# Kernel optimization log

Measured on AMD Instinct MI355X. Metric: run time of the kernel, lower is better.

## Reference

```python
import jax, jax.numpy as jnp
import numpy as np

MARGIN = 0.3   # init margin
NUMBER = 1024  # OHEM: number of hardest losses to mine
N, D = 8192, 128


def setup_inputs() -> dict:
    key = jax.random.key(0)
    k1, k2 = jax.random.split(key)
    pair1 = jax.random.normal(k1, (N, D), dtype=jnp.float32)
    pair2 = jax.random.normal(k2, (N, D), dtype=jnp.float32)
    return {"pair1": pair1, "pair2": pair2}


def _pairwise_losses(pair1, pair2):
    # d[i, j] = ||pair1[i] - pair2[j]||^2 via GEMM expansion
    sq1 = jnp.sum(pair1 * pair1, axis=1)            # [N]
    sq2 = jnp.sum(pair2 * pair2, axis=1)            # [N]
    cross = pair1 @ pair2.T                          # [N, N]
    d = sq1[:, None] + sq2[None, :] - 2.0 * cross    # [N, N]
    dist_ap = jnp.diagonal(d)                        # [N], ||pair1[i]-pair2[i]||^2
    loss = jax.nn.relu(dist_ap[:, None] - d + MARGIN)  # [N, N]
    offdiag = ~jnp.eye(d.shape[0], dtype=bool)       # i == j is skipped
    return loss, offdiag


def reference(pair1, pair2):
    loss, offdiag = _pairwise_losses(pair1, pair2)
    n = loss.shape[0]
    cnt = 2 * n * (n - 1)  # original appends each (i, j) loss twice
    # all_loss: mean over all 2*N*(N-1) (duplicated) losses
    all_loss = 2.0 * jnp.sum(jnp.where(offdiag, loss, 0.0)) / cnt
    # OHEM: top NUMBER losses over the duplicated candidate set
    flat = jnp.where(offdiag, loss, -1.0).ravel()    # sentinel -1 masks diagonal
    flat2 = jnp.concatenate([flat, flat])            # each loss appears twice
    topv, _ = jax.lax.top_k(flat2, NUMBER)
    pos = topv > 0.0
    avg_num = jnp.sum(pos)
    avg_sum = jnp.sum(jnp.where(pos, topv, 0.0))
    # if no positive loss among the mined set, fall back to the single largest loss
    avg_loss = jnp.where(avg_num > 0, avg_sum / jnp.maximum(avg_num, 1).astype(topv.dtype), topv[0])
    return avg_loss, all_loss
```

## Files before the change

kernel.cpp:

```cpp
#include <hip/hip_runtime.h>
#include <stdint.h>


#define NROWS 8192
#define DDIM  128
#define MARGIN_F 0.3f
#define HALFK 512
#define SUBCAP 8192
#define SHIST_BINS 1024

typedef unsigned short u16;
typedef short bf16x8 __attribute__((ext_vector_type(8)));
typedef float f32x4 __attribute__((ext_vector_type(4)));

#define OFF_P1B  0
#define OFF_P2B  (2*1024*1024)
#define OFF_AARR (4*1024*1024)
#define OFF_BARR (OFF_AARR + 32768)
#define OFF_MISC (OFF_AARR + 65536)
#define OFF_CAND (OFF_MISC + 8192)

__global__ void init_kernel(int* zbase) {
    const int n = 1232;
    for (int i = threadIdx.x; i < n; i += blockDim.x) zbase[i] = 0;
}

__device__ __forceinline__ u16 f2bf(float f) {
    unsigned int u = __float_as_uint(f);
    u = (u + 0x7FFFu + ((u >> 16) & 1u)) >> 16;
    return (u16)u;
}
__device__ __forceinline__ float bf2f(u16 u) {
    return __uint_as_float(((unsigned int)u) << 16);
}

__global__ __launch_bounds__(256) void prep_kernel(
    const float* __restrict__ p1, const float* __restrict__ p2,
    u16* __restrict__ p1b, u16* __restrict__ p2b,
    float* __restrict__ aArr, float* __restrict__ bArr)
{
    const int wid = threadIdx.x >> 6, lane = threadIdx.x & 63;
    const int row = blockIdx.x*4 + wid;
    const float2 v1 = *(const float2*)&p1[row*DDIM + lane*2];
    const float2 v2 = *(const float2*)&p2[row*DDIM + lane*2];
    p1b[row*DDIM + lane*2]     = f2bf(v1.x);
    p1b[row*DDIM + lane*2 + 1] = f2bf(v1.y);
    p2b[row*DDIM + lane*2]     = f2bf(v2.x);
    p2b[row*DDIM + lane*2 + 1] = f2bf(v2.y);
    float sq = v2.x*v2.x + v2.y*v2.y;
    float cp = v1.x*v2.x + v1.y*v2.y;
    #pragma unroll
    for (int off = 32; off > 0; off >>= 1) {
        sq += __shfl_down(sq, off);
        cp += __shfl_down(cp, off);
    }
    if (lane == 0) {
        bArr[row] = sq;
        aArr[row] = sq - 2.0f*cp + MARGIN_F;
    }
}

__global__ __launch_bounds__(256) void sample_kernel(
    const u16* __restrict__ p1b, const u16* __restrict__ p2b,
    const float* __restrict__ aArr, const float* __restrict__ bArr,
    int* __restrict__ shist)
{
    __shared__ float p1row[DDIM];
    __shared__ int h[SHIST_BINS];
    const int b = blockIdx.x;
    const int i = (b >> 3)*1024 + 512;
    const int j0 = (b & 7)*1024;
    const int tid = threadIdx.x;
    for (int k = tid; k < SHIST_BINS; k += 256) h[k] = 0;
    if (tid < DDIM) p1row[tid] = bf2f(p1b[i*DDIM + tid]);
    __syncthreads();
    const float ai = aArr[i];
    #pragma unroll
    for (int jj = 0; jj < 4; ++jj) {
        const int j = j0 + jj*256 + tid;
        const u16* prow = &p2b[j*DDIM];
        float dot = 0.f;
        for (int k = 0; k < DDIM; k += 8) {
            uint4 q = *(const uint4*)&prow[k];
            const u16* e = (const u16*)&q;
            #pragma unroll
            for (int t = 0; t < 8; ++t) dot += p1row[k + t] * bf2f(e[t]);
        }
        float v = ai - bArr[j] + 2.0f*dot;
        if (j != i && v > 0.f) {
            int bin = (int)(v * 4.0f);
            if (bin > SHIST_BINS - 1) bin = SHIST_BINS - 1;
            atomicAdd(&h[bin], 1);
        }
    }
    __syncthreads();
    for (int k = tid; k < SHIST_BINS; k += 256) if (h[k]) atomicAdd(&shist[k], h[k]);
}

__global__ void pick_kernel(const int* __restrict__ shist, float* __restrict__ Tv) {
    if (threadIdx.x == 0) {
        int run = 0, b;
        float t = 0.f;
        for (b = SHIST_BINS - 1; b >= 0; --b) { run += shist[b]; if (run >= 8) break; }
        if (run >= 8) {
            if (b < 0) b = 0;
            while (run > 24 && run - shist[b] >= 8 && b < SHIST_BINS - 1) { run -= shist[b]; b++; }
            t = 0.25f * (float)b;
        }
        *Tv = t;
    }
}

__global__ __launch_bounds__(256, 2) void pair_gemm(
    const u16* __restrict__ p1b, const u16* __restrict__ p2b,
    const float* __restrict__ aArr, const float* __restrict__ bArr,
    const float* __restrict__ Tv,
    float* __restrict__ pS, int* __restrict__ pP,
    int* __restrict__ candCnt, float* __restrict__ cand)
{
    __shared__ u16 At[128][136];
    __shared__ u16 Bt[128][136];
    __shared__ float sredS[4];
    __shared__ int   sredP[4];
    const int tid = threadIdx.x;
    const int bi = blockIdx.y, bj = blockIdx.x;
    const int i0 = bi*128, j0 = bj*128;
    const float T0 = *Tv;
    #pragma unroll
    for (int it = 0; it < 8; ++it) {
        int c = tid + it*256;
        int r = c >> 4, cc = (c & 15) * 8;
        *(uint4*)&At[r][cc] = *(const uint4*)&p1b[(i0 + r)*DDIM + cc];
        *(uint4*)&Bt[r][cc] = *(const uint4*)&p2b[(j0 + r)*DDIM + cc];
    }
    __syncthreads();
    const int lane = tid & 63, wid = tid >> 6;
    const int r16 = lane & 15, hi = lane >> 4;
    const int wm = (wid >> 1)*64, wn = (wid & 1)*64;
    f32x4 acc[4][4];
    #pragma unroll
    for (int a = 0; a < 4; ++a)
        #pragma unroll
        for (int b = 0; b < 4; ++b) acc[a][b] = (f32x4){0.f, 0.f, 0.f, 0.f};
    #pragma unroll
    for (int ks = 0; ks < 4; ++ks) {
        const int kc = ks*32 + hi*8;
        bf16x8 aF[4], bF[4];
        #pragma unroll
        for (int mi = 0; mi < 4; ++mi) aF[mi] = *(const bf16x8*)&At[wm + mi*16 + r16][kc];
        #pragma unroll
        for (int ni = 0; ni < 4; ++ni) bF[ni] = *(const bf16x8*)&Bt[wn + ni*16 + r16][kc];
        #pragma unroll
        for (int mi = 0; mi < 4; ++mi)
            #pragma unroll
            for (int ni = 0; ni < 4; ++ni)
                acc[mi][ni] = __builtin_amdgcn_mfma_f32_16x16x32_bf16(aF[mi], bF[ni], acc[mi][ni], 0, 0, 0);
    }
    float bv[4], av[4][4];
    #pragma unroll
    for (int ni = 0; ni < 4; ++ni) bv[ni] = bArr[j0 + wn + ni*16 + r16];
    #pragma unroll
    for (int mi = 0; mi < 4; ++mi)
        #pragma unroll
        for (int r = 0; r < 4; ++r) av[mi][r] = aArr[i0 + wm + mi*16 + hi*4 + r];
    const int copy = (bi ^ bj) & 63;
    int*   myCnt  = &candCnt[copy];
    float* myCand = &cand[(size_t)copy * SUBCAP];
    float lsum = 0.f; int pcnt = 0;
    #pragma unroll
    for (int mi = 0; mi < 4; ++mi) {
        #pragma unroll
        for (int ni = 0; ni < 4; ++ni) {
            const bool hasDiag = (i0 + wm + mi*16) == (j0 + wn + ni*16);
            #pragma unroll
            for (int r = 0; r < 4; ++r) {
                const float v = av[mi][r] - bv[ni] + 2.0f*acc[mi][ni][r];
                lsum += fmaxf(v, 0.f);
                pcnt += (v > 0.f) ? 1 : 0;
                bool ok = (v >= T0);
                if (hasDiag && (hi*4 + r) == r16) ok = false;
                if (ok) {
                    int idx = atomicAdd(myCnt, 1);
                    if (idx < SUBCAP) myCand[idx] = v;
                }
            }
        }
    }
    #pragma unroll
    for (int off = 32; off > 0; off >>= 1) {
        lsum += __shfl_down(lsum, off);
        pcnt += __shfl_down(pcnt, off);
    }
    if (lane == 0) { sredS[wid] = lsum; sredP[wid] = pcnt; }
    __syncthreads();
    if (tid == 0) {
        atomicAdd(&pS[copy], sredS[0] + sredS[1] + sredS[2] + sredS[3]);
        atomicAdd(&pP[copy], sredP[0] + sredP[1] + sredP[2] + sredP[3]);
    }
}

__device__ __forceinline__ float block_reduce1024(float v, float* red, int tid) {
    #pragma unroll
    for (int off = 32; off > 0; off >>= 1) v += __shfl_down(v, off);
    __syncthreads();
    if ((tid & 63) == 0) red[tid >> 6] = v;
    __syncthreads();
    if (tid == 0) {
        float t = 0.f;
        #pragma unroll
        for (int w = 0; w < 16; ++w) t += red[w];
        red[0] = t;
    }
    __syncthreads();
    return red[0];
}

__global__ __launch_bounds__(1024) void select_kernel(
    const float* __restrict__ pS, const int* __restrict__ pP,
    const int* __restrict__ candCnt, const float* __restrict__ cand,
    const float* __restrict__ Tv, float* __restrict__ out)
{
    __shared__ int h1[1024];
    __shared__ int h2[1024];
    __shared__ float red[16];
    __shared__ int ints[8];
    __shared__ float fl[2];
    __shared__ float lst[4096];
    const int tid = threadIdx.x;
    for (int k = tid; k < 1024; k += 1024) { h1[k] = 0; h2[k] = 0; }
    if (tid == 0) {
        double sd = 0.0; int p = 0, c = 0;
        for (int k = 0; k < 64; ++k) {
            sd += (double)pS[k];
            p += pP[k];
            int cc = candCnt[k];
            c += (cc > SUBCAP ? SUBCAP : cc);
        }
        sd -= (double)NROWS * (double)MARGIN_F;
        if (sd < 0.0) sd = 0.0;
        p -= NROWS;
        if (p < 0) p = 0;
        ints[0] = p; ints[1] = c; ints[6] = 0;
        fl[0] = (float)sd;
    }
    __syncthreads();
    const int P = ints[0], C = ints[1];
    const float S = fl[0];
    const float all_loss = S * (1.0f / 67100672.0f);
    const float lo = *Tv;
    float avg = 0.f;

    if (P == 0) {
        avg = 0.f;
    } else if (P < HALFK) {
        avg = S / (float)P;
    } else if (C < HALFK) {
        float s = 0.f;
        for (int c = 0; c < 64; ++c) {
            int n = min(candCnt[c], SUBCAP);
            for (int k = tid; k < n; k += 1024) s += cand[(size_t)c*SUBCAP + k];
        }
        s = block_reduce1024(s, red, tid);
        avg = (C > 0) ? (s + (float)(HALFK - C)*lo) / (float)HALFK : 0.f;
    } else {
        for (int c = 0; c < 64; ++c) {
            int n = min(candCnt[c], SUBCAP);
            for (int k = tid; k < n; k += 1024) {
                float v = cand[(size_t)c*SUBCAP + k];
                int b = (int)((v - lo) * 0.25f);
                b = b < 0 ? 0 : (b > 1023 ? 1023 : b);
                atomicAdd(&h1[b], 1);
            }
        }
        __syncthreads();
        if (tid == 0) {
            int run = 0;
            for (int b = 1023; b >= 0; --b) {
                run += h1[b];
                if (run >= HALFK) { ints[2] = b; ints[3] = HALFK - (run - h1[b]); break; }
            }
        }
        __syncthreads();
        const int b1 = ints[2], needK = ints[3];
        const float lo2 = lo + (float)b1 * 4.0f;
        float s1 = 0.f;
        for (int c = 0; c < 64; ++c) {
            int n = min(candCnt[c], SUBCAP);
            for (int k = tid; k < n; k += 1024) {
                float v = cand[(size_t)c*SUBCAP + k];
                int b = (int)((v - lo) * 0.25f);
                b = b < 0 ? 0 : (b > 1023 ? 1023 : b);
                if (b > b1) s1 += v;
                else if (b == b1) {
                    int sb = (int)((v - lo2) * 256.0f);
                    sb = sb < 0 ? 0 : (sb > 1023 ? 1023 : sb);
                    atomicAdd(&h2[sb], 1);
                }
            }
        }
        s1 = block_reduce1024(s1, red, tid);
        if (tid == 0) {
            int run = 0;
            for (int b = 1023; b >= 0; --b) {
                run += h2[b];
                if (run >= needK) { ints[4] = b; ints[5] = needK - (run - h2[b]); break; }
            }
        }
        __syncthreads();
        const int b2 = ints[4], need3 = ints[5];
        float s2 = 0.f;
        for (int c = 0; c < 64; ++c) {
            int n = min(candCnt[c], SUBCAP);
            for (int k = tid; k < n; k += 1024) {
                float v = cand[(size_t)c*SUBCAP + k];
                int b = (int)((v - lo) * 0.25f);
                b = b < 0 ? 0 : (b > 1023 ? 1023 : b);
                if (b == b1) {
                    int sb = (int)((v - lo2) * 256.0f);
                    sb = sb < 0 ? 0 : (sb > 1023 ? 1023 : sb);
                    if (sb > b2) s2 += v;
                    else if (sb == b2) {
                        int idx = atomicAdd(&ints[6], 1);
                        if (idx < 4096) lst[idx] = v;
                    }
                }
            }
        }
        s2 = block_reduce1024(s2, red, tid);
        __syncthreads();
        const int m = min(ints[6], 4096);
        float s3 = 0.f;
        for (int k = tid; k < m; k += 1024) {
            float v = lst[k]; int g = 0;
            for (int j = 0; j < m; ++j) {
                float u = lst[j];
                g += (u > v) || (u == v && j < k);
            }
            if (g < need3) s3 += v;
        }
        s3 = block_reduce1024(s3, red, tid);
        avg = (s1 + s2 + s3) * (1.0f / (float)HALFK);
    }
    if (tid == 0) { out[0] = avg; out[1] = all_loss; }
}

extern "C" void kernel_launch(void* const* d_in, const int* in_sizes, int n_in,
                              void* d_out, int out_size, void* d_ws, size_t ws_size,
                              hipStream_t stream)
{
    const float* p1 = (const float*)d_in[0];
    const float* p2 = (const float*)d_in[1];
    char* ws = (char*)d_ws;
    u16*   p1b  = (u16*)(ws + OFF_P1B);
    u16*   p2b  = (u16*)(ws + OFF_P2B);
    float* aArr = (float*)(ws + OFF_AARR);
    float* bArr = (float*)(ws + OFF_BARR);
    int*   misc = (int*)(ws + OFF_MISC);
    int*   shist = misc;
    float* pS   = (float*)(misc + 1024);
    int*   pP   = misc + 1088;
    int*   cCnt = misc + 1152;
    float* Tv   = (float*)(misc + 1216);
    float* cand = (float*)(ws + OFF_CAND);
    float* out  = (float*)d_out;

    init_kernel<<<1, 256, 0, stream>>>(misc);
    prep_kernel<<<NROWS/4, 256, 0, stream>>>(p1, p2, p1b, p2b, aArr, bArr);
    sample_kernel<<<64, 256, 0, stream>>>(p1b, p2b, aArr, bArr, shist);
    pick_kernel<<<1, 64, 0, stream>>>(shist, Tv);
    dim3 grid(64, 64);
    pair_gemm<<<grid, 256, 0, stream>>>(p1b, p2b, aArr, bArr, Tv, pS, pP, cCnt, cand);
    select_kernel<<<1, 1024, 0, stream>>>(pS, pP, cCnt, cand, Tv, out);
}
```

Baseline: 401.8 us.

## Split pair GEMM into candidate and sum kernels; use wave-aggregated atomics

After: 425.2 us. 5.8% more time.

```diff
diff --git a/kernel.cpp b/kernel.cpp
--- a/kernel.cpp
+++ b/kernel.cpp
@@ -97,26 +97,117 @@
     for (int k = tid; k < SHIST_BINS; k += 256) if (h[k]) atomicAdd(&shist[k], h[k]);
 }
 
-__global__ void pick_kernel(const int* __restrict__ shist, float* __restrict__ Tv) {
-    if (threadIdx.x == 0) {
-        int run = 0, b;
-        float t = 0.f;
-        for (b = SHIST_BINS - 1; b >= 0; --b) { run += shist[b]; if (run >= 8) break; }
-        if (run >= 8) {
-            if (b < 0) b = 0;
-            while (run > 24 && run - shist[b] >= 8 && b < SHIST_BINS - 1) { run -= shist[b]; b++; }
-            t = 0.25f * (float)b;
-        }
-        *Tv = t;
-    }
-}
-
-__global__ __launch_bounds__(256, 2) void pair_gemm(
+__global__ __launch_bounds__(256) void pick_kernel(
+    const int* __restrict__ shist, float* __restrict__ Tv)
+{
+    __shared__ int h[SHIST_BINS];
+    __shared__ int chunk[256];
+    const int tid = threadIdx.x;
+    #pragma unroll
+    for (int k = 0; k < 4; ++k) h[tid + k*256] = shist[tid + k*256];
+    __syncthreads();
+    int cs = 0;
+    #pragma unroll
+    for (int k = 0; k < 4; ++k) cs += h[tid*4 + k];
+    chunk[tid] = cs;
+    __syncthreads();
+    if (tid == 0) {
+        int run = 0, tc = -1;
+        for (int t = 255; t >= 0; --t) {
+            if (run + chunk[t] >= 8) { tc = t; break; }
+            run += chunk[t];
+        }
+        float t0 = 0.f;
+        if (tc >= 0) {
+            int b = tc*4 + 3;
+            for (; b >= tc*4; --b) { run += h[b]; if (run >= 8) break; }
+            if (b < tc*4) b = tc*4;
+            while (run > 24 && run - h[b] >= 8 && b < SHIST_BINS - 1) { run -= h[b]; b++; }
+            t0 = 0.25f * (float)b;
+        }
+        *Tv = t0;
+    }
+}
+
+__global__ __launch_bounds__(256, 2) void gemm_cand(
     const u16* __restrict__ p1b, const u16* __restrict__ p2b,
     const float* __restrict__ aArr, const float* __restrict__ bArr,
     const float* __restrict__ Tv,
-    float* __restrict__ pS, int* __restrict__ pP,
     int* __restrict__ candCnt, float* __restrict__ cand)
+{
+    __shared__ u16 At[128][136];
+    __shared__ u16 Bt[128][136];
+    const int tid = threadIdx.x;
+    const int bi = blockIdx.y, bj = blockIdx.x;
+    const int i0 = bi*128, j0 = bj*128;
+    const float T0 = *Tv;
+    #pragma unroll
+    for (int it = 0; it < 8; ++it) {
+        int c = tid + it*256;
+        int r = c >> 4, cc = (c & 15) * 8;
+        *(uint4*)&At[r][cc] = *(const uint4*)&p1b[(i0 + r)*DDIM + cc];
+        *(uint4*)&Bt[r][cc] = *(const uint4*)&p2b[(j0 + r)*DDIM + cc];
+    }
+    __syncthreads();
+    const int lane = tid & 63, wid = tid >> 6;
+    const int r16 = lane & 15, hi = lane >> 4;
+    const int wm = (wid >> 1)*64, wn = (wid & 1)*64;
+    f32x4 acc[4][4];
+    #pragma unroll
+    for (int a = 0; a < 4; ++a)
+        #pragma unroll
+        for (int b = 0; b < 4; ++b) acc[a][b] = (f32x4){0.f, 0.f, 0.f, 0.f};
+    #pragma unroll
+    for (int ks = 0; ks < 4; ++ks) {
+        const int kc = ks*32 + hi*8;
+        bf16x8 aF[4], bF[4];
+        #pragma unroll
+        for (int mi = 0; mi < 4; ++mi) aF[mi] = *(const bf16x8*)&At[wm + mi*16 + r16][kc];
+        #pragma unroll
+        for (int ni = 0; ni < 4; ++ni) bF[ni] = *(const bf16x8*)&Bt[wn + ni*16 + r16][kc];
+        #pragma unroll
+        for (int mi = 0; mi < 4; ++mi)
+            #pragma unroll
+            for (int ni = 0; ni < 4; ++ni)
+                acc[mi][ni] = __builtin_amdgcn_mfma_f32_16x16x32_bf16(aF[mi], bF[ni], acc[mi][ni], 0, 0, 0);
+    }
+    float bv[4], av[4][4];
+    #pragma unroll
+    for (int ni = 0; ni < 4; ++ni) bv[ni] = bArr[j0 + wn + ni*16 + r16];
+    #pragma unroll
+    for (int mi = 0; mi < 4; ++mi)
+        #pragma unroll
+        for (int r = 0; r < 4; ++r) av[mi][r] = aArr[i0 + wm + mi*16 + hi*4 + r];
+    const int copy = (bi ^ bj) & 63;
+    #pragma unroll
+    for (int mi = 0; mi < 4; ++mi) {
+        #pragma unroll
+        for (int ni = 0; ni < 4; ++ni) {
+            #pragma unroll
+            for (int r = 0; r < 4; ++r) {
+                const int ii = i0 + wm + mi*16 + hi*4 + r;
+                const int jj = j0 + wn + ni*16 + r16;
+                const float v = av[mi][r] - bv[ni] + 2.0f*acc[mi][ni][r];
+                const bool cd = (v > 0.f) && (ii != jj) && (v >= T0);
+                unsigned long long m = __ballot(cd);
+                if (m) {
+                    int base = 0;
+                    if (lane == 0) base = atomicAdd(&candCnt[copy], __popcll(m));
+                    base = __shfl(base, 0);
+                    if (cd) {
+                        int pos = base + __popcll(m & ((1ULL << lane) - 1));
+                        if (pos < SUBCAP) cand[(size_t)copy*SUBCAP + pos] = v;
+                    }
+                }
+            }
+        }
+    }
+}
+
+__global__ __launch_bounds__(256, 2) void gemm_sum(
+    const u16* __restrict__ p1b, const u16* __restrict__ p2b,
+    const float* __restrict__ aArr, const float* __restrict__ bArr,
+    float* __restrict__ pS, int* __restrict__ pP)
 {
     __shared__ u16 At[128][136];
     __shared__ u16 Bt[128][136];
@@ -125,7 +216,6 @@
     const int tid = threadIdx.x;
     const int bi = blockIdx.y, bj = blockIdx.x;
     const int i0 = bi*128, j0 = bj*128;
-    const float T0 = *Tv;
     #pragma unroll
     for (int it = 0; it < 8; ++it) {
         int c = tid + it*256;
@@ -163,29 +253,22 @@
     for (int mi = 0; mi < 4; ++mi)
         #pragma unroll
         for (int r = 0; r < 4; ++r) av[mi][r] = aArr[i0 + wm + mi*16 + hi*4 + r];
-    const int copy = (bi ^ bj) & 63;
-    int*   myCnt  = &candCnt[copy];
-    float* myCand = &cand[(size_t)copy * SUBCAP];
-    float lsum = 0.f; int pcnt = 0;
+    float ls[4] = {0.f, 0.f, 0.f, 0.f};
+    int   pc[4] = {0, 0, 0, 0};
     #pragma unroll
     for (int mi = 0; mi < 4; ++mi) {
         #pragma unroll
         for (int ni = 0; ni < 4; ++ni) {
-            const bool hasDiag = (i0 + wm + mi*16) == (j0 + wn + ni*16);
             #pragma unroll
             for (int r = 0; r < 4; ++r) {
                 const float v = av[mi][r] - bv[ni] + 2.0f*acc[mi][ni][r];
-                lsum += fmaxf(v, 0.f);
-                pcnt += (v > 0.f) ? 1 : 0;
-                bool ok = (v >= T0);
-                if (hasDiag && (hi*4 + r) == r16) ok = false;
-                if (ok) {
-                    int idx = atomicAdd(myCnt, 1);
-                    if (idx < SUBCAP) myCand[idx] = v;
-                }
-            }
-        }
-    }
+                ls[r] += fmaxf(v, 0.f);
+                pc[r] += (v > 0.f) ? 1 : 0;
+            }
+        }
+    }
+    float lsum = (ls[0] + ls[1]) + (ls[2] + ls[3]);
+    int   pcnt = (pc[0] + pc[1]) + (pc[2] + pc[3]);
     #pragma unroll
     for (int off = 32; off > 0; off >>= 1) {
         lsum += __shfl_down(lsum, off);
@@ -194,6 +277,7 @@
     if (lane == 0) { sredS[wid] = lsum; sredP[wid] = pcnt; }
     __syncthreads();
     if (tid == 0) {
+        const int copy = (bi ^ bj) & 63;
         atomicAdd(&pS[copy], sredS[0] + sredS[1] + sredS[2] + sredS[3]);
         atomicAdd(&pP[copy], sredP[0] + sredP[1] + sredP[2] + sredP[3]);
     }
@@ -367,8 +451,9 @@
     init_kernel<<<1, 256, 0, stream>>>(misc);
     prep_kernel<<<NROWS/4, 256, 0, stream>>>(p1, p2, p1b, p2b, aArr, bArr);
     sample_kernel<<<64, 256, 0, stream>>>(p1b, p2b, aArr, bArr, shist);
-    pick_kernel<<<1, 64, 0, stream>>>(shist, Tv);
+    pick_kernel<<<1, 256, 0, stream>>>(shist, Tv);
     dim3 grid(64, 64);
-    pair_gemm<<<grid, 256, 0, stream>>>(p1b, p2b, aArr, bArr, Tv, pS, pP, cCnt, cand);
+    gemm_cand<<<grid, 256, 0, stream>>>(p1b, p2b, aArr, bArr, Tv, cCnt, cand);
+    gemm_sum<<<grid, 256, 0, stream>>>(p1b, p2b, aArr, bArr, pS, pP);
     select_kernel<<<1, 1024, 0, stream>>>(pS, pP, cCnt, cand, Tv, out);
 }
```

## Restructure pairwise GEMM to register-resident B tile streaming A rows without LDS

Applied to the files above, without the earlier changes.

New measurement: 527.1 us. +31.2%, slower.

```diff
diff --git a/kernel.cpp b/kernel.cpp
--- a/kernel.cpp
+++ b/kernel.cpp
@@ -97,105 +97,138 @@
     for (int k = tid; k < SHIST_BINS; k += 256) if (h[k]) atomicAdd(&shist[k], h[k]);
 }
 
-__global__ void pick_kernel(const int* __restrict__ shist, float* __restrict__ Tv) {
-    if (threadIdx.x == 0) {
-        int run = 0, b;
-        float t = 0.f;
-        for (b = SHIST_BINS - 1; b >= 0; --b) { run += shist[b]; if (run >= 8) break; }
-        if (run >= 8) {
-            if (b < 0) b = 0;
-            while (run > 24 && run - shist[b] >= 8 && b < SHIST_BINS - 1) { run -= shist[b]; b++; }
-            t = 0.25f * (float)b;
-        }
-        *Tv = t;
-    }
-}
-
-__global__ __launch_bounds__(256, 2) void pair_gemm(
+__global__ __launch_bounds__(256) void pick_kernel(
+    const int* __restrict__ shist, float* __restrict__ Tv)
+{
+    __shared__ int h[SHIST_BINS];
+    __shared__ int chunk[256];
+    const int tid = threadIdx.x;
+    #pragma unroll
+    for (int k = 0; k < 4; ++k) h[tid + k*256] = shist[tid + k*256];
+    __syncthreads();
+    int cs = 0;
+    #pragma unroll
+    for (int k = 0; k < 4; ++k) cs += h[tid*4 + k];
+    chunk[tid] = cs;
+    __syncthreads();
+    if (tid == 0) {
+        int run = 0, tc = -1;
+        for (int t = 255; t >= 0; --t) {
+            if (run + chunk[t] >= 8) { tc = t; break; }
+            run += chunk[t];
+        }
+        float t0 = 0.f;
+        if (tc >= 0) {
+            int b = tc*4 + 3;
+            for (; b >= tc*4; --b) { run += h[b]; if (run >= 8) break; }
+            if (b < tc*4) b = tc*4;
+            while (run > 24 && run - h[b] >= 8 && b < SHIST_BINS - 1) { run -= h[b]; b++; }
+            t0 = 0.25f * (float)b;
+        }
+        *Tv = t0;
+    }
+}
+
+__global__ __launch_bounds__(512, 2) void pair_main(
     const u16* __restrict__ p1b, const u16* __restrict__ p2b,
     const float* __restrict__ aArr, const float* __restrict__ bArr,
     const float* __restrict__ Tv,
     float* __restrict__ pS, int* __restrict__ pP,
     int* __restrict__ candCnt, float* __restrict__ cand)
 {
-    __shared__ u16 At[128][136];
-    __shared__ u16 Bt[128][136];
-    __shared__ float sredS[4];
-    __shared__ int   sredP[4];
     const int tid = threadIdx.x;
-    const int bi = blockIdx.y, bj = blockIdx.x;
-    const int i0 = bi*128, j0 = bj*128;
+    const int w = tid >> 6, lane = tid & 63;
+    const int r16 = lane & 15, hi = lane >> 4;
+    const int j0 = blockIdx.x * 64;
+    const int ibase = blockIdx.y * 2048;
     const float T0 = *Tv;
-    #pragma unroll
-    for (int it = 0; it < 8; ++it) {
-        int c = tid + it*256;
-        int r = c >> 4, cc = (c & 15) * 8;
-        *(uint4*)&At[r][cc] = *(const uint4*)&p1b[(i0 + r)*DDIM + cc];
-        *(uint4*)&Bt[r][cc] = *(const uint4*)&p2b[(j0 + r)*DDIM + cc];
-    }
-    __syncthreads();
-    const int lane = tid & 63, wid = tid >> 6;
-    const int r16 = lane & 15, hi = lane >> 4;
-    const int wm = (wid >> 1)*64, wn = (wid & 1)*64;
-    f32x4 acc[4][4];
-    #pragma unroll
-    for (int a = 0; a < 4; ++a)
-        #pragma unroll
-        for (int b = 0; b < 4; ++b) acc[a][b] = (f32x4){0.f, 0.f, 0.f, 0.f};
-    #pragma unroll
-    for (int ks = 0; ks < 4; ++ks) {
-        const int kc = ks*32 + hi*8;
-        bf16x8 aF[4], bF[4];
-        #pragma unroll
-        for (int mi = 0; mi < 4; ++mi) aF[mi] = *(const bf16x8*)&At[wm + mi*16 + r16][kc];
-        #pragma unroll
-        for (int ni = 0; ni < 4; ++ni) bF[ni] = *(const bf16x8*)&Bt[wn + ni*16 + r16][kc];
-        #pragma unroll
-        for (int mi = 0; mi < 4; ++mi)
+    const char* Ap = (const char*)p1b;
+    const char* Bp = (const char*)p2b;
+
+    bf16x8 bF[4][4];
+    #pragma unroll
+    for (int ni = 0; ni < 4; ++ni) {
+        const int j = j0 + ni*16 + r16;
+        #pragma unroll
+        for (int ks = 0; ks < 4; ++ks)
+            bF[ni][ks] = *(const bf16x8*)(Bp + (size_t)j*256 + hi*16 + ks*64);
+    }
+    float bv[4];
+    int jj[4];
+    #pragma unroll
+    for (int ni = 0; ni < 4; ++ni) {
+        jj[ni] = j0 + ni*16 + r16;
+        bv[ni] = bArr[jj[ni]];
+    }
+
+    float ls[4] = {0.f, 0.f, 0.f, 0.f};
+    int pcnt = 0;
+    const int copy = (blockIdx.x*8 + w) & 63;
+    int*   myCnt  = &candCnt[copy];
+    float* myCand = &cand[(size_t)copy * SUBCAP];
+
+    const int row0 = ibase + w*256;
+
+    bf16x8 aCur[4];
+    float avCur[4];
+    #pragma unroll
+    for (int ks = 0; ks < 4; ++ks)
+        aCur[ks] = *(const bf16x8*)(Ap + (size_t)(row0 + r16)*256 + hi*16 + ks*64);
+    #pragma unroll
+    for (int r = 0; r < 4; ++r) avCur[r] = aArr[row0 + hi*4 + r];
+
+    #pragma unroll
+    for (int t = 0; t < 16; ++t) {
+        bf16x8 aNxt[4];
+        float avNxt[4];
+        if (t < 15) {
+            const int rn = row0 + (t + 1)*16;
+            #pragma unroll
+            for (int ks = 0; ks < 4; ++ks)
+                aNxt[ks] = *(const bf16x8*)(Ap + (size_t)(rn + r16)*256 + hi*16 + ks*64);
+            #pragma unroll
+            for (int r = 0; r < 4; ++r) avNxt[r] = aArr[rn + hi*4 + r];
+        }
+        f32x4 acc[4];
+        #pragma unroll
+        for (int ni = 0; ni < 4; ++ni) acc[ni] = (f32x4){0.f, 0.f, 0.f, 0.f};
+        #pragma unroll
+        for (int ks = 0; ks < 4; ++ks)
             #pragma unroll
             for (int ni = 0; ni < 4; ++ni)
-                acc[mi][ni] = __builtin_amdgcn_mfma_f32_16x16x32_bf16(aF[mi], bF[ni], acc[mi][ni], 0, 0, 0);
-    }
-    float bv[4], av[4][4];
-    #pragma unroll
-    for (int ni = 0; ni < 4; ++ni) bv[ni] = bArr[j0 + wn + ni*16 + r16];
-    #pragma unroll
-    for (int mi = 0; mi < 4; ++mi)
-        #pragma unroll
-        for (int r = 0; r < 4; ++r) av[mi][r] = aArr[i0 + wm + mi*16 + hi*4 + r];
-    const int copy = (bi ^ bj) & 63;
-    int*   myCnt  = &candCnt[copy];
-    float* myCand = &cand[(size_t)copy * SUBCAP];
-    float lsum = 0.f; int pcnt = 0;
-    #pragma unroll
-    for (int mi = 0; mi < 4; ++mi) {
+                acc[ni] = __builtin_amdgcn_mfma_f32_16x16x32_bf16(aCur[ks], bF[ni][ks], acc[ni], 0, 0, 0);
+        const int rr = row0 + t*16;
+        const int iL = rr + hi*4;
         #pragma unroll
         for (int ni = 0; ni < 4; ++ni) {
-            const bool hasDiag = (i0 + wm + mi*16) == (j0 + wn + ni*16);
             #pragma unroll
             for (int r = 0; r < 4; ++r) {
-                const float v = av[mi][r] - bv[ni] + 2.0f*acc[mi][ni][r];
-                lsum += fmaxf(v, 0.f);
+                const float v = avCur[r] - bv[ni] + 2.0f*acc[ni][r];
+                ls[ni] += fmaxf(v, 0.f);
                 pcnt += (v > 0.f) ? 1 : 0;
-                bool ok = (v >= T0);
-                if (hasDiag && (hi*4 + r) == r16) ok = false;
-                if (ok) {
+                const bool isD = (iL + r) == jj[ni];
+                const float vc = isD ? -1e30f : v;
+                if (vc >= T0) {
                     int idx = atomicAdd(myCnt, 1);
                     if (idx < SUBCAP) myCand[idx] = v;
                 }
             }
         }
-    }
+        #pragma unroll
+        for (int ks = 0; ks < 4; ++ks) aCur[ks] = aNxt[ks];
+        #pragma unroll
+        for (int r = 0; r < 4; ++r) avCur[r] = avNxt[r];
+    }
+
+    float lsum = (ls[0] + ls[1]) + (ls[2] + ls[3]);
     #pragma unroll
     for (int off = 32; off > 0; off >>= 1) {
         lsum += __shfl_down(lsum, off);
         pcnt += __shfl_down(pcnt, off);
     }
-    if (lane == 0) { sredS[wid] = lsum; sredP[wid] = pcnt; }
-    __syncthreads();
-    if (tid == 0) {
-        atomicAdd(&pS[copy], sredS[0] + sredS[1] + sredS[2] + sredS[3]);
-        atomicAdd(&pP[copy], sredP[0] + sredP[1] + sredP[2] + sredP[3]);
+    if (lane == 0) {
+        atomicAdd(&pS[copy], lsum);
+        atomicAdd(&pP[copy], pcnt);
     }
 }
 
@@ -367,8 +400,8 @@
     init_kernel<<<1, 256, 0, stream>>>(misc);
     prep_kernel<<<NROWS/4, 256, 0, stream>>>(p1, p2, p1b, p2b, aArr, bArr);
     sample_kernel<<<64, 256, 0, stream>>>(p1b, p2b, aArr, bArr, shist);
-    pick_kernel<<<1, 64, 0, stream>>>(shist, Tv);
-    dim3 grid(64, 64);
-    pair_gemm<<<grid, 256, 0, stream>>>(p1b, p2b, aArr, bArr, Tv, pS, pP, cCnt, cand);
+    pick_kernel<<<1, 256, 0, stream>>>(shist, Tv);
+    dim3 grid(128, 4);
+    pair_main<<<grid, 512, 0, stream>>>(p1b, p2b, aArr, bArr, Tv, pS, pP, cCnt, cand);
     select_kernel<<<1, 1024, 0, stream>>>(pS, pP, cCnt, cand, Tv, out);
 }
```

## Enlarge pair GEMM tile to 256x256 with 512 threads and parallelize threshold pick

Applied to the files above, without the earlier changes.

Measured after the change: 382.4 us. -4.8%, faster.

```diff
diff --git a/kernel.cpp b/kernel.cpp
--- a/kernel.cpp
+++ b/kernel.cpp
@@ -97,38 +97,56 @@
     for (int k = tid; k < SHIST_BINS; k += 256) if (h[k]) atomicAdd(&shist[k], h[k]);
 }
 
-__global__ void pick_kernel(const int* __restrict__ shist, float* __restrict__ Tv) {
-    if (threadIdx.x == 0) {
-        int run = 0, b;
-        float t = 0.f;
-        for (b = SHIST_BINS - 1; b >= 0; --b) { run += shist[b]; if (run >= 8) break; }
-        if (run >= 8) {
-            if (b < 0) b = 0;
-            while (run > 24 && run - shist[b] >= 8 && b < SHIST_BINS - 1) { run -= shist[b]; b++; }
-            t = 0.25f * (float)b;
-        }
-        *Tv = t;
-    }
-}
-
-__global__ __launch_bounds__(256, 2) void pair_gemm(
+__global__ __launch_bounds__(256) void pick_kernel(
+    const int* __restrict__ shist, float* __restrict__ Tv)
+{
+    __shared__ int h[SHIST_BINS];
+    __shared__ int chunk[256];
+    const int tid = threadIdx.x;
+    #pragma unroll
+    for (int k = 0; k < 4; ++k) h[tid + k*256] = shist[tid + k*256];
+    __syncthreads();
+    int cs = 0;
+    #pragma unroll
+    for (int k = 0; k < 4; ++k) cs += h[tid*4 + k];
+    chunk[tid] = cs;
+    __syncthreads();
+    if (tid == 0) {
+        int run = 0, tc = -1;
+        for (int t = 255; t >= 0; --t) {
+            if (run + chunk[t] >= 8) { tc = t; break; }
+            run += chunk[t];
+        }
+        float t0 = 0.f;
+        if (tc >= 0) {
+            int b = tc*4 + 3;
+            for (; b >= tc*4; --b) { run += h[b]; if (run >= 8) break; }
+            if (b < tc*4) b = tc*4;
+            while (run > 24 && run - h[b] >= 8 && b < SHIST_BINS - 1) { run -= h[b]; b++; }
+            t0 = 0.25f * (float)b;
+        }
+        *Tv = t0;
+    }
+}
+
+__global__ __launch_bounds__(512, 1) void pair_gemm(
     const u16* __restrict__ p1b, const u16* __restrict__ p2b,
     const float* __restrict__ aArr, const float* __restrict__ bArr,
     const float* __restrict__ Tv,
     float* __restrict__ pS, int* __restrict__ pP,
     int* __restrict__ candCnt, float* __restrict__ cand)
 {
-    __shared__ u16 At[128][136];
-    __shared__ u16 Bt[128][136];
-    __shared__ float sredS[4];
-    __shared__ int   sredP[4];
+    __shared__ u16 At[256][136];
+    __shared__ u16 Bt[256][136];
+    __shared__ float sredS[8];
+    __shared__ int   sredP[8];
     const int tid = threadIdx.x;
     const int bi = blockIdx.y, bj = blockIdx.x;
-    const int i0 = bi*128, j0 = bj*128;
+    const int i0 = bi*256, j0 = bj*256;
     const float T0 = *Tv;
     #pragma unroll
     for (int it = 0; it < 8; ++it) {
-        int c = tid + it*256;
+        int c = tid + it*512;
         int r = c >> 4, cc = (c & 15) * 8;
         *(uint4*)&At[r][cc] = *(const uint4*)&p1b[(i0 + r)*DDIM + cc];
         *(uint4*)&Bt[r][cc] = *(const uint4*)&p2b[(j0 + r)*DDIM + cc];
@@ -136,56 +154,64 @@
     __syncthreads();
     const int lane = tid & 63, wid = tid >> 6;
     const int r16 = lane & 15, hi = lane >> 4;
-    const int wm = (wid >> 1)*64, wn = (wid & 1)*64;
-    f32x4 acc[4][4];
-    #pragma unroll
-    for (int a = 0; a < 4; ++a)
-        #pragma unroll
-        for (int b = 0; b < 4; ++b) acc[a][b] = (f32x4){0.f, 0.f, 0.f, 0.f};
-    #pragma unroll
-    for (int ks = 0; ks < 4; ++ks) {
-        const int kc = ks*32 + hi*8;
-        bf16x8 aF[4], bF[4];
-        #pragma unroll
-        for (int mi = 0; mi < 4; ++mi) aF[mi] = *(const bf16x8*)&At[wm + mi*16 + r16][kc];
-        #pragma unroll
-        for (int ni = 0; ni < 4; ++ni) bF[ni] = *(const bf16x8*)&Bt[wn + ni*16 + r16][kc];
-        #pragma unroll
-        for (int mi = 0; mi < 4; ++mi)
-            #pragma unroll
-            for (int ni = 0; ni < 4; ++ni)
-                acc[mi][ni] = __builtin_amdgcn_mfma_f32_16x16x32_bf16(aF[mi], bF[ni], acc[mi][ni], 0, 0, 0);
-    }
-    float bv[4], av[4][4];
-    #pragma unroll
-    for (int ni = 0; ni < 4; ++ni) bv[ni] = bArr[j0 + wn + ni*16 + r16];
-    #pragma unroll
-    for (int mi = 0; mi < 4; ++mi)
-        #pragma unroll
-        for (int r = 0; r < 4; ++r) av[mi][r] = aArr[i0 + wm + mi*16 + hi*4 + r];
-    const int copy = (bi ^ bj) & 63;
+    const int wr = (wid >> 2) * 128;
+    const int wc = (wid & 3) * 64;
+    const int copy = (bi*5 + bj) & 63;
     int*   myCnt  = &candCnt[copy];
     float* myCand = &cand[(size_t)copy * SUBCAP];
+    float bv[4];
+    #pragma unroll
+    for (int ni = 0; ni < 4; ++ni) bv[ni] = bArr[j0 + wc + ni*16 + r16];
     float lsum = 0.f; int pcnt = 0;
-    #pragma unroll
-    for (int mi = 0; mi < 4; ++mi) {
-        #pragma unroll
-        for (int ni = 0; ni < 4; ++ni) {
-            const bool hasDiag = (i0 + wm + mi*16) == (j0 + wn + ni*16);
-            #pragma unroll
-            for (int r = 0; r < 4; ++r) {
-                const float v = av[mi][r] - bv[ni] + 2.0f*acc[mi][ni][r];
-                lsum += fmaxf(v, 0.f);
-                pcnt += (v > 0.f) ? 1 : 0;
-                bool ok = (v >= T0);
-                if (hasDiag && (hi*4 + r) == r16) ok = false;
-                if (ok) {
-                    int idx = atomicAdd(myCnt, 1);
-                    if (idx < SUBCAP) myCand[idx] = v;
+
+    #pragma unroll
+    for (int h = 0; h < 2; ++h) {
+        const int rbase = wr + h*64;
+        f32x4 acc[4][4];
+        #pragma unroll
+        for (int a = 0; a < 4; ++a)
+            #pragma unroll
+            for (int b = 0; b < 4; ++b) acc[a][b] = (f32x4){0.f, 0.f, 0.f, 0.f};
+        #pragma unroll
+        for (int ks = 0; ks < 4; ++ks) {
+            const int kc = ks*32 + hi*8;
+            bf16x8 aF[4], bF[4];
+            #pragma unroll
+            for (int mi = 0; mi < 4; ++mi) aF[mi] = *(const bf16x8*)&At[rbase + mi*16 + r16][kc];
+            #pragma unroll
+            for (int ni = 0; ni < 4; ++ni) bF[ni] = *(const bf16x8*)&Bt[wc + ni*16 + r16][kc];
+            #pragma unroll
+            for (int mi = 0; mi < 4; ++mi)
+                #pragma unroll
+                for (int ni = 0; ni < 4; ++ni)
+                    acc[mi][ni] = __builtin_amdgcn_mfma_f32_16x16x32_bf16(aF[mi], bF[ni], acc[mi][ni], 0, 0, 0);
+        }
+        float av[4][4];
+        #pragma unroll
+        for (int mi = 0; mi < 4; ++mi)
+            #pragma unroll
+            for (int r = 0; r < 4; ++r) av[mi][r] = aArr[i0 + rbase + mi*16 + hi*4 + r];
+        #pragma unroll
+        for (int mi = 0; mi < 4; ++mi) {
+            #pragma unroll
+            for (int ni = 0; ni < 4; ++ni) {
+                const bool hasDiag = (i0 + rbase + mi*16) == (j0 + wc + ni*16);
+                #pragma unroll
+                for (int r = 0; r < 4; ++r) {
+                    const float v = av[mi][r] - bv[ni] + 2.0f*acc[mi][ni][r];
+                    lsum += fmaxf(v, 0.f);
+                    pcnt += (v > 0.f) ? 1 : 0;
+                    bool ok = (v >= T0);
+                    if (hasDiag && (hi*4 + r) == r16) ok = false;
+                    if (ok) {
+                        int idx = atomicAdd(myCnt, 1);
+                        if (idx < SUBCAP) myCand[idx] = v;
+                    }
                 }
             }
         }
     }
+
     #pragma unroll
     for (int off = 32; off > 0; off >>= 1) {
         lsum += __shfl_down(lsum, off);
@@ -194,8 +220,11 @@
     if (lane == 0) { sredS[wid] = lsum; sredP[wid] = pcnt; }
     __syncthreads();
     if (tid == 0) {
-        atomicAdd(&pS[copy], sredS[0] + sredS[1] + sredS[2] + sredS[3]);
-        atomicAdd(&pP[copy], sredP[0] + sredP[1] + sredP[2] + sredP[3]);
+        float s = 0.f; int p = 0;
+        #pragma unroll
+        for (int w = 0; w < 8; ++w) { s += sredS[w]; p += sredP[w]; }
+        atomicAdd(&pS[copy], s);
+        atomicAdd(&pP[copy], p);
     }
 }
 
@@ -367,8 +396,8 @@
     init_kernel<<<1, 256, 0, stream>>>(misc);
     prep_kernel<<<NROWS/4, 256, 0, stream>>>(p1, p2, p1b, p2b, aArr, bArr);
     sample_kernel<<<64, 256, 0, stream>>>(p1b, p2b, aArr, bArr, shist);
-    pick_kernel<<<1, 64, 0, stream>>>(shist, Tv);
-    dim3 grid(64, 64);
-    pair_gemm<<<grid, 256, 0, stream>>>(p1b, p2b, aArr, bArr, Tv, pS, pP, cCnt, cand);
+    pick_kernel<<<1, 256, 0, stream>>>(shist, Tv);
+    dim3 grid(32, 32);
+    pair_gemm<<<grid, 512, 0, stream>>>(p1b, p2b, aArr, bArr, Tv, pS, pP, cCnt, cand);
     select_kernel<<<1, 1024, 0, stream>>>(pS, pP, cCnt, cand, Tv, out);
 }
```
